# Kernel optimization log

Measured on AMD Instinct MI355X. Metric: run time of the kernel, lower is better.

The kernel has to match this reference:

```python
import jax, jax.numpy as jnp
import numpy as np
from jax import lax

K = 3
STRIDE = 1
PAD = 1


def setup_inputs() -> dict:
    key = jax.random.key(0)
    k1, k2, k3, k4 = jax.random.split(key, 4)
    x = jax.random.normal(k1, (8, 64, 128, 128), dtype=jnp.float32)
    # offset conv params (trained-state stand-in; module inits to 0, which is degenerate)
    w_off = jax.random.normal(k2, (2 * K * K, 64, K, K), dtype=jnp.float32) * 0.01
    b_off = jax.random.normal(k3, (2 * K * K,), dtype=jnp.float32) * 0.01
    w_dcn = jax.random.normal(k4, (64, 64, K, K), dtype=jnp.float32) * 0.05
    return {"x": x, "w_off": w_off, "b_off": b_off, "w_dcn": w_dcn}


def _deform_conv(x, offset, weight):
    # x: [B,C,H,W]; offset: [B,2*K*K,Ho,Wo] interleaved (dy,dx) per kernel tap;
    # weight: [Cout,Cin,K,K]. Matches torchvision.ops.deform_conv2d semantics (groups=1).
    B, C, H, W = x.shape
    Cout = weight.shape[0]
    KK = K * K
    Ho = (H + 2 * PAD - K) // STRIDE + 1
    Wo = (W + 2 * PAD - K) // STRIDE + 1
    off = offset.reshape(B, KK, 2, Ho, Wo)
    ky = (jnp.arange(KK) // K).astype(x.dtype)
    kx = (jnp.arange(KK) % K).astype(x.dtype)
    base_y = (jnp.arange(Ho) * STRIDE - PAD).astype(x.dtype)
    base_x = (jnp.arange(Wo) * STRIDE - PAD).astype(x.dtype)
    # sampling coords per (batch, kernel tap, output y, output x)
    py = base_y[None, None, :, None] + ky[None, :, None, None] + off[:, :, 0]  # [B,KK,Ho,Wo]
    px = base_x[None, None, None, :] + kx[None, :, None, None] + off[:, :, 1]
    y0 = jnp.floor(py)
    x0 = jnp.floor(px)
    dy = py - y0
    dx = px - x0
    y0i = y0.astype(jnp.int32)
    x0i = x0.astype(jnp.int32)
    flat = x.reshape(B, C, H * W)

    def gather(yi, xi):
        valid = (yi >= 0) & (yi < H) & (xi >= 0) & (xi < W)
        idx = (jnp.clip(yi, 0, H - 1) * W + jnp.clip(xi, 0, W - 1)).reshape(B, -1)
        g = jax.vmap(lambda f, i: f[:, i])(flat, idx)  # [B,C,KK*Ho*Wo]
        return g.reshape(B, C, KK, Ho, Wo) * valid.reshape(B, 1, KK, Ho, Wo).astype(x.dtype)

    w00 = ((1 - dy) * (1 - dx))[:, None]  # [B,1,KK,Ho,Wo]
    w01 = ((1 - dy) * dx)[:, None]
    w10 = (dy * (1 - dx))[:, None]
    w11 = (dy * dx)[:, None]
    vals = (gather(y0i, x0i) * w00 + gather(y0i, x0i + 1) * w01
            + gather(y0i + 1, x0i) * w10 + gather(y0i + 1, x0i + 1) * w11)
    return jnp.einsum('bckhw,ock->bohw', vals, weight.reshape(Cout, C, KK))


def reference(x, w_off, b_off, w_dcn):
    offset = lax.conv_general_dilated(
        x, w_off, window_strides=(STRIDE, STRIDE),
        padding=((PAD, PAD), (PAD, PAD)),
        dimension_numbers=('NCHW', 'OIHW', 'NCHW')) + b_off[None, :, None, None]
    return _deform_conv(x, offset, w_dcn)
```

## Files before the change

### kernel.cpp

```cpp
#include <hip/hip_runtime.h>
#include <cmath>

#define BATCH 8
#define CIN   64
#define HH    128
#define WW    128
#define COUT  64
#define KKT   9
#define NOFF  18
#define PIX   16
#define NPX   32
#define KTOT  576
#define WROWS 6
#define WCOLS 24
#define NSAMP (NPX*KKT)
#define KH3   192

typedef __bf16 bf16x8 __attribute__((ext_vector_type(8)));
typedef float  f32x4  __attribute__((ext_vector_type(4)));
typedef float  f32x2  __attribute__((ext_vector_type(2)));
typedef unsigned int u32;
typedef u32    u32x4  __attribute__((ext_vector_type(4)));

__device__ __bf16 g_wb[18 * 4 * 4 * 16 * 8];
__device__ __bf16 g_wboff[18 * 2 * 4 * 16 * 8];

__global__ __launch_bounds__(256)
void prep_w(const float* __restrict__ w_dcn, const float* __restrict__ w_off) {
    const int idx = blockIdx.x * 256 + threadIdx.x;
    if (idx < 18 * 4 * 4 * 16 * 8) {
        const int e  = idx & 7;
        const int lr = (idx >> 3) & 15;
        const int lg = (idx >> 7) & 3;
        const int w  = (idx >> 9) & 3;
        const int kb = idx >> 11;
        const int cout = w * 16 + lr;
        const int k  = kb * 32 + lg * 8 + e;
        const int kk = k >> 6, ci = k & 63;
        g_wb[idx] = (__bf16)w_dcn[cout * KTOT + ci * KKT + kk];
    } else {
        const int j  = idx - 18 * 4 * 4 * 16 * 8;
        const int e  = j & 7;
        const int lr = (j >> 3) & 15;
        const int lg = (j >> 7) & 3;
        const int nt = (j >> 9) & 1;
        const int kb = j >> 10;
        const int oc = nt * 16 + lr;
        const int k  = kb * 32 + lg * 8 + e;
        const int kk = k >> 6, ci = k & 63;
        g_wboff[j] = (oc < NOFF) ? (__bf16)w_off[oc * KTOT + ci * KKT + kk] : (__bf16)0.f;
    }
}

static __device__ __forceinline__ f32x2 unpk(u32 v) {
    f32x2 r;
    r.x = __builtin_bit_cast(float, v << 16);
    r.y = __builtin_bit_cast(float, v & 0xffff0000u);
    return r;
}

static __device__ __forceinline__ u32 pkbf(float a, float b) {
    const u32 lo = (u32)__builtin_bit_cast(unsigned short, (__bf16)a);
    const u32 hi = (u32)__builtin_bit_cast(unsigned short, (__bf16)b);
    return lo | (hi << 16);
}

__global__ __launch_bounds__(256)
void deform_fused(const float* __restrict__ x,
                  const float* __restrict__ b_off,
                  float* __restrict__ out) {
    __shared__ __align__(16) __bf16 s_xw[WROWS * WCOLS * 64];
    __shared__ __align__(16) __bf16 s_vals[NPX * KH3];
    __shared__ float s_off[NPX * NOFF];
    __shared__ int   s_meta[NSAMP];
    __shared__ int   s_yx[NSAMP];
    __shared__ float s_bw[NSAMP][4];

    const int blk   = blockIdx.x;
    const int wtile = blk % (WW / PIX);
    const int r0    = ((blk / (WW / PIX)) % (HH / 2)) * 2;
    const int b     = blk / ((WW / PIX) * (HH / 2));
    const int wbase = wtile * PIX;
    const int tid   = threadIdx.x;
    const int wid   = tid >> 6;
    const int lane  = tid & 63;
    const int lr    = lane & 15;
    const int lg    = lane >> 4;

    const float* __restrict__ xb = x + (size_t)b * CIN * HH * WW;
    const bool interior = (r0 >= 2) & (r0 <= HH - 4) & (wtile >= 1) & (wtile <= (WW / PIX) - 2);

    for (int t = tid; t < 6 * 32 * WROWS; t += 256) {
        const int c   = t % 6;
        const int cp  = (t / 6) & 31;
        const int yr  = t / 192;
        const int ci0 = cp * 2;
        const int y   = r0 - 2 + yr;
        const int xs  = wbase - 4 + c * 4;
        f32x4 va = {0.f, 0.f, 0.f, 0.f};
        f32x4 vb = {0.f, 0.f, 0.f, 0.f};
        if (interior) {
            const float* __restrict__ rp = xb + (size_t)ci0 * (HH * WW) + y * WW + xs;
            va = *(const f32x4*)rp;
            vb = *(const f32x4*)(rp + HH * WW);
        } else if (y >= 0 && y < HH) {
            const float* __restrict__ rp = xb + (size_t)ci0 * (HH * WW) + y * WW + xs;
            if (xs >= 0 && xs <= WW - 4) {
                va = *(const f32x4*)rp;
                vb = *(const f32x4*)(rp + HH * WW);
            } else {
                #pragma unroll
                for (int dx = 0; dx < 4; ++dx) {
                    if (xs + dx >= 0 && xs + dx < WW) {
                        va[dx] = rp[dx];
                        vb[dx] = rp[dx + HH * WW];
                    }
                }
            }
        }
        const int eb = ((yr * WCOLS + c * 4) << 6) + ci0;
        #pragma unroll
        for (int dx = 0; dx < 4; ++dx) {
            const int elem = (eb + (dx << 6)) ^ (((c * 4 + dx) & 7) << 3);
            *(u32*)&s_xw[elem] = pkbf(va[dx], vb[dx]);
        }
    }
    __syncthreads();

    {
        const int pg = wid >> 1;
        const int nt = wid & 1;
        f32x4 acc = {0.f, 0.f, 0.f, 0.f};
        #pragma unroll
        for (int kb = 0; kb < 18; ++kb) {
            const int kbase = kb * 32 + lg * 8;
            const int kk    = kbase >> 6;
            const int ci0   = kbase & 63;
            const int yr    = pg + kk / 3 + 1;
            const int xr    = lr + kk % 3 + 3;
            const int elem  = (((yr * WCOLS + xr) << 6) + ci0) ^ ((xr & 7) << 3);
            const bf16x8 a  = *(const bf16x8*)&s_xw[elem];
            const bf16x8 bb = *(const bf16x8*)&g_wboff[(((kb * 2 + nt) * 4 + lg) * 16 + lr) * 8];
            acc = __builtin_amdgcn_mfma_f32_16x16x32_bf16(a, bb, acc, 0, 0, 0);
        }
        const int oc = nt * 16 + lr;
        if (oc < NOFF) {
            const float bias = b_off[oc];
            #pragma unroll
            for (int r = 0; r < 4; ++r)
                s_off[(pg * 16 + lg * 4 + r) * NOFF + oc] = acc[r] + bias;
        }
    }
    __syncthreads();

    for (int m = tid; m < NSAMP; m += 256) {
        const int p  = m / KKT;
        const int kk = m - p * KKT;
        const int hp = r0 + (p >> 4);
        const int wo = wbase + (p & 15);
        const float py = (float)(hp - 1 + kk / 3) + s_off[p * NOFF + 2 * kk + 0];
        const float px = (float)(wo - 1 + kk % 3) + s_off[p * NOFF + 2 * kk + 1];
        const float fy = floorf(py), fx = floorf(px);
        const int y0 = (int)fy, x0 = (int)fx;
        const float dy = py - fy, dx = px - fx;
        const int yr = y0 - (r0 - 2);
        const int xr = x0 - (wbase - 4);
        const int fast = (yr >= 0) & (yr <= 4) & (xr >= 0) & (xr <= 22);
        const u32 rowidx = (u32)(yr * WCOLS + xr);
        s_meta[m] = fast ? (int)(0x80000000u | (rowidx << 16)
                                 | (((u32)(xr & 7) << 3) << 8)
                                 | ((u32)((xr + 1) & 7) << 3))
                         : 0;
        s_yx[m] = (y0 << 16) | (x0 & 0xffff);
        s_bw[m][0] = (1.f - dy) * (1.f - dx);
        s_bw[m][1] = (1.f - dy) * dx;
        s_bw[m][2] = dy * (1.f - dx);
        s_bw[m][3] = dy * dx;
    }
    __syncthreads();

    auto run_task = [&](int m, int p, int kkl, int c8) {
        const int meta = s_meta[m];
        const f32x4 w = *(const f32x4*)&s_bw[m][0];
        bf16x8 o;
        if (meta < 0) {
            const u32 um  = (u32)meta;
            const int r6  = (int)((um >> 16) & 0xffu) << 6;
            const int sw0 = (int)((um >> 8) & 0xffu);
            const int sw1 = (int)(um & 0xffu);
            const int a0  = r6 + (c8 ^ sw0);
            const int a1  = r6 + 64 + (c8 ^ sw1);
            const u32x4 u00 = *(const u32x4*)&s_xw[a0];
            const u32x4 u01 = *(const u32x4*)&s_xw[a1];
            const u32x4 u10 = *(const u32x4*)&s_xw[a0 + WCOLS * 64];
            const u32x4 u11 = *(const u32x4*)&s_xw[a1 + WCOLS * 64];
            #pragma unroll
            for (int u = 0; u < 4; ++u) {
                f32x2 a = unpk(u00[u]) * w[0];
                a += unpk(u01[u]) * w[1];
                a += unpk(u10[u]) * w[2];
                a += unpk(u11[u]) * w[3];
                o[2 * u + 0] = (__bf16)a.x;
                o[2 * u + 1] = (__bf16)a.y;
            }
        } else {
            const int yx = s_yx[m];
            const int y0 = yx >> 16;
            const int x0 = (int)(short)(yx & 0xffff);
            const int y1 = y0 + 1, x1 = x0 + 1;
            #pragma unroll
            for (int e = 0; e < 8; ++e) {
                const float* __restrict__ xc = xb + (size_t)(c8 + e) * (HH * WW);
                float v = 0.f;
                if (y0 >= 0 && y0 < HH) {
                    if (x0 >= 0 && x0 < WW) v += xc[y0 * WW + x0] * w[0];
                    if (x1 >= 0 && x1 < WW) v += xc[y0 * WW + x1] * w[1];
                }
                if (y1 >= 0 && y1 < HH) {
                    if (x0 >= 0 && x0 < WW) v += xc[y1 * WW + x0] * w[2];
                    if (x1 >= 0 && x1 < WW) v += xc[y1 * WW + x1] * w[3];
                }
                o[e] = (__bf16)v;
            }
        }
        const int ew = (kkl * 64 + c8) ^ ((p & 7) << 3);
        *(bf16x8*)&s_vals[p * KH3 + ew] = o;
    };

    f32x4 acc0 = {0.f, 0.f, 0.f, 0.f};
    f32x4 acc1 = {0.f, 0.f, 0.f, 0.f};
    const __bf16* __restrict__ bsrc = g_wb + (((size_t)wid * 4 + lg) * 16 + lr) * 8;

    #pragma unroll 1
    for (int pass = 0; pass < 3; ++pass) {
        for (int t = tid; t < 768; t += 256) {
            const int s3 = t >> 3, c8 = (t & 7) << 3;
            const int p = s3 / 3, kkl = s3 - p * 3;
            run_task(p * KKT + pass * 3 + kkl, p, kkl, c8);
        }
        __syncthreads();
        #pragma unroll
        for (int j = 0; j < 6; ++j) {
            const int kb = pass * 6 + j;
            const int ew = (j * 32 + lg * 8) ^ ((lr & 7) << 3);
            const bf16x8 bf = *(const bf16x8*)(bsrc + (size_t)kb * 2048);
            const bf16x8 a0 = *(const bf16x8*)&s_vals[lr * KH3 + ew];
            const bf16x8 a1 = *(const bf16x8*)&s_vals[(16 + lr) * KH3 + ew];
            acc0 = __builtin_amdgcn_mfma_f32_16x16x32_bf16(a0, bf, acc0, 0, 0, 0);
            acc1 = __builtin_amdgcn_mfma_f32_16x16x32_bf16(a1, bf, acc1, 0, 0, 0);
        }
        if (pass < 2) __syncthreads();
    }

    const int cout = wid * 16 + lr;
    const size_t ob0 = (((size_t)b * COUT + cout) * HH + r0) * WW + wbase + lg * 4;
    *(f32x4*)&out[ob0]      = acc0;
    *(f32x4*)&out[ob0 + WW] = acc1;
}

extern "C" void kernel_launch(void* const* d_in, const int* in_sizes, int n_in,
                              void* d_out, int out_size, void* d_ws, size_t ws_size,
                              hipStream_t stream) {
    const float* x     = (const float*)d_in[0];
    const float* w_off = (const float*)d_in[1];
    const float* b_off = (const float*)d_in[2];
    const float* w_dcn = (const float*)d_in[3];
    float* out = (float*)d_out;

    prep_w<<<216, 256, 0, stream>>>(w_dcn, w_off);

    const int nblocks = BATCH * (HH / 2) * (WW / PIX);
    deform_fused<<<nblocks, 256, 0, stream>>>(x, b_off, out);
}
```

Baseline: 64.78 us.

## Repartition MFMA work across waves with split-K and LDS reduction

Each wave previously handled 16 output channels for all 32 pixels. Now each wave handles 16 pixels and all 64 channels, with the K dimension split across wave pairs and the partial sums combined through shared memory. Each A fragment is reused across four MFMAs, and each wave issues fewer LDS A loads. The cost is more global B loads per wave, an extra reduction step with two more barriers, and output stores done by only half the waves.

```diff
diff --git a/kernel.cpp b/kernel.cpp
--- a/kernel.cpp
+++ b/kernel.cpp
@@ -227,9 +227,12 @@
         *(bf16x8*)&s_vals[p * KH3 + ew] = o;
     };
 
-    f32x4 acc0 = {0.f, 0.f, 0.f, 0.f};
-    f32x4 acc1 = {0.f, 0.f, 0.f, 0.f};
-    const __bf16* __restrict__ bsrc = g_wb + (((size_t)wid * 4 + lg) * 16 + lr) * 8;
+    const int pg5 = wid >> 1;
+    const int kh  = wid & 1;
+    const int pix = pg5 * 16 + lr;
+
+    f32x4 acc[4] = {{0.f,0.f,0.f,0.f}, {0.f,0.f,0.f,0.f},
+                    {0.f,0.f,0.f,0.f}, {0.f,0.f,0.f,0.f}};
 
     #pragma unroll 1
     for (int pass = 0; pass < 3; ++pass) {
@@ -240,22 +243,43 @@
         }
         __syncthreads();
         #pragma unroll
-        for (int j = 0; j < 6; ++j) {
+        for (int jj = 0; jj < 3; ++jj) {
+            const int j  = kh * 3 + jj;
             const int kb = pass * 6 + j;
             const int ew = (j * 32 + lg * 8) ^ ((lr & 7) << 3);
-            const bf16x8 bf = *(const bf16x8*)(bsrc + (size_t)kb * 2048);
-            const bf16x8 a0 = *(const bf16x8*)&s_vals[lr * KH3 + ew];
-            const bf16x8 a1 = *(const bf16x8*)&s_vals[(16 + lr) * KH3 + ew];
-            acc0 = __builtin_amdgcn_mfma_f32_16x16x32_bf16(a0, bf, acc0, 0, 0, 0);
-            acc1 = __builtin_amdgcn_mfma_f32_16x16x32_bf16(a1, bf, acc1, 0, 0, 0);
+            const bf16x8 a = *(const bf16x8*)&s_vals[pix * KH3 + ew];
+            const __bf16* __restrict__ bp = g_wb + (size_t)kb * 2048 + lg * 128 + lr * 8;
+            #pragma unroll
+            for (int t4 = 0; t4 < 4; ++t4)
+                acc[t4] = __builtin_amdgcn_mfma_f32_16x16x32_bf16(
+                    a, *(const bf16x8*)(bp + t4 * 512), acc[t4], 0, 0, 0);
         }
         if (pass < 2) __syncthreads();
     }
-
-    const int cout = wid * 16 + lr;
-    const size_t ob0 = (((size_t)b * COUT + cout) * HH + r0) * WW + wbase + lg * 4;
-    *(f32x4*)&out[ob0]      = acc0;
-    *(f32x4*)&out[ob0 + WW] = acc1;
+    __syncthreads();
+
+    f32x4* red = (f32x4*)s_xw;
+    if (kh == 1) {
+        const int base = (pg5 * 64 + lane) * 5;
+        red[base + 0] = acc[0];
+        red[base + 1] = acc[1];
+        red[base + 2] = acc[2];
+        red[base + 3] = acc[3];
+    }
+    __syncthreads();
+    if (kh == 0) {
+        const int base = (pg5 * 64 + lane) * 5;
+        acc[0] += red[base + 0];
+        acc[1] += red[base + 1];
+        acc[2] += red[base + 2];
+        acc[3] += red[base + 3];
+        const size_t orow = ((size_t)b * COUT + lr) * HH + r0 + pg5;
+        const size_t ocol = wbase + lg * 4;
+        *(f32x4*)&out[(orow +  0 * (size_t)HH) * WW + ocol] = acc[0];
+        *(f32x4*)&out[(orow + 16 * (size_t)HH) * WW + ocol] = acc[1];
+        *(f32x4*)&out[(orow + 32 * (size_t)HH) * WW + ocol] = acc[2];
+        *(f32x4*)&out[(orow + 48 * (size_t)HH) * WW + ocol] = acc[3];
+    }
 }
 
 extern "C" void kernel_launch(void* const* d_in, const int* in_sizes, int n_in,
```

Result: slower. 71.28 us (+10.0%).
